# Performance work log

Hardware: AMD Instinct MI355X
Metric: run time of the kernel (lower is better)

## Reference

```python
import jax, jax.numpy as jnp
import numpy as np

VOCAB, EMBED, HIDDEN = 32000, 1024, 1024
BATCH, SEQ = 64, 128
PAD_IDX = 0


def setup_inputs() -> dict:
    key = jax.random.key(0)
    k_in, k_emb, k_wih, k_whh, k_bih, k_bhh = jax.random.split(key, 6)
    inputs = jax.random.randint(k_in, (BATCH, SEQ), 0, VOCAB)
    emb = jax.random.normal(k_emb, (VOCAB, EMBED), dtype=jnp.float32)
    emb = emb.at[PAD_IDX].set(0.0)  # nn.Embedding zeros the padding_idx row
    s = 1.0 / np.sqrt(HIDDEN).astype(np.float32)  # torch LSTMCell init bound
    W_ih = jax.random.uniform(k_wih, (4 * HIDDEN, EMBED), minval=-s, maxval=s, dtype=jnp.float32)
    W_hh = jax.random.uniform(k_whh, (4 * HIDDEN, HIDDEN), minval=-s, maxval=s, dtype=jnp.float32)
    b_ih = jax.random.uniform(k_bih, (4 * HIDDEN,), minval=-s, maxval=s, dtype=jnp.float32)
    b_hh = jax.random.uniform(k_bhh, (4 * HIDDEN,), minval=-s, maxval=s, dtype=jnp.float32)
    return {"emb": emb, "W_ih": W_ih, "W_hh": W_hh, "b_ih": b_ih, "b_hh": b_hh, "inputs": inputs}


def reference(emb, W_ih, W_hh, b_ih, b_hh, inputs):
    # Embedding lookup: [B, S, E] -> time-major [S, B, E]
    x = jnp.swapaxes(emb[inputs], 0, 1)
    B = inputs.shape[0]
    H = W_hh.shape[1]
    h0 = jnp.zeros((B, H), dtype=emb.dtype)
    c0 = jnp.zeros((B, H), dtype=emb.dtype)

    def step(carry, xt):
        h, c = carry
        # torch LSTMCell gate order: i, f, g, o
        gates = xt @ W_ih.T + b_ih + h @ W_hh.T + b_hh  # [B, 4H]
        i, f, g, o = jnp.split(gates, 4, axis=-1)
        i = jax.nn.sigmoid(i)
        f = jax.nn.sigmoid(f)
        g = jnp.tanh(g)
        o = jax.nn.sigmoid(o)
        c2 = f * c + i * g
        h2 = o * jnp.tanh(c2)
        # NOTE: original's h_c_mask is all-zeros (its fill loop only writes
        # zeros), so torch.where always selects the new state -> no masking.
        return (h2, c2), None

    (h, c), _ = jax.lax.scan(step, (h0, c0), x)
    return (h, c)
```

## Files before the change

### kernel.cpp

```cpp
#include <hip/hip_runtime.h>
#include <hip/hip_bf16.h>

#define EMB   1024
#define HID   1024
#define NBATCH 64
#define SEQ   128
#define NGATE 4096
#define NBLK  128

typedef __attribute__((ext_vector_type(8))) short bf16x8;
typedef __attribute__((ext_vector_type(4))) float f32x4;

__device__ __forceinline__ unsigned short f2bf(float f) {
    unsigned int u = __float_as_uint(f);
    unsigned int r = (u + 0x7FFFu + ((u >> 16) & 1u)) >> 16;
    return (unsigned short)r;
}

__device__ __forceinline__ bf16x8 pack8(float4 a, float4 b) {
    bf16x8 r;
    r[0] = (short)f2bf(a.x); r[1] = (short)f2bf(a.y);
    r[2] = (short)f2bf(a.z); r[3] = (short)f2bf(a.w);
    r[4] = (short)f2bf(b.x); r[5] = (short)f2bf(b.y);
    r[6] = (short)f2bf(b.z); r[7] = (short)f2bf(b.w);
    return r;
}

__device__ __forceinline__ float sigmoidf_(float x) { return 1.0f / (1.0f + __expf(-x)); }
__device__ __forceinline__ float tanhf_(float x)    { return 1.0f - 2.0f / (1.0f + __expf(2.0f * x)); }


__global__ void gather_x(const float* __restrict__ emb, const int* __restrict__ inp,
                         unsigned short* __restrict__ xbf) {
    int m = blockIdx.x;
    int t = m >> 6, b = m & 63;
    int tok = inp[b * SEQ + t];
    float4 v = ((const float4*)(emb + (long)tok * EMB))[threadIdx.x];
    ushort4 o;
    o.x = f2bf(v.x); o.y = f2bf(v.y); o.z = f2bf(v.z); o.w = f2bf(v.w);
    ((ushort4*)(xbf + (long)m * EMB))[threadIdx.x] = o;
}

__global__ void conv_w(const float* __restrict__ w, unsigned short* __restrict__ wbf) {
    long i = (long)blockIdx.x * 1024 + (long)threadIdx.x * 4;
    float4 v = *(const float4*)(w + i);
    ushort4 o;
    o.x = f2bf(v.x); o.y = f2bf(v.y); o.z = f2bf(v.z); o.w = f2bf(v.w);
    *(ushort4*)(wbf + i) = o;
}

__global__ void bsum_k(const float* __restrict__ bi, const float* __restrict__ bh,
                       float* __restrict__ bs) {
    int i = blockIdx.x * 256 + threadIdx.x;
    bs[i] = bi[i] + bh[i];
}

__global__ __launch_bounds__(256) void gemm_xw(const unsigned short* __restrict__ A,
                                               const unsigned short* __restrict__ Bw,
                                               const float* __restrict__ bsum,
                                               float* __restrict__ XW) {
    __shared__ unsigned short As[128][40];
    __shared__ unsigned short Bs[128][40];
    int bx = blockIdx.x;
    int by = blockIdx.y;
    int tid = threadIdx.x;
    int w = tid >> 6, l = tid & 63;
    int wm = w >> 1, wn = w & 1;
    int lr = l & 15, lk = l >> 4;

    f32x4 acc[4][4];
#pragma unroll
    for (int ni = 0; ni < 4; ++ni) {
        float bsv = bsum[bx * 128 + wn * 64 + ni * 16 + lr];
#pragma unroll
        for (int mi = 0; mi < 4; ++mi) {
            acc[mi][ni][0] = bsv; acc[mi][ni][1] = bsv;
            acc[mi][ni][2] = bsv; acc[mi][ni][3] = bsv;
        }
    }

    int sr = tid >> 1;
    int sc = (tid & 1) * 16;
    const unsigned short* ga = A  + (long)(by * 128 + sr) * 1024 + sc;
    const unsigned short* gb = Bw + (long)(bx * 128 + sr) * 1024 + sc;

    for (int kt = 0; kt < 32; ++kt) {
        uint4 va0 = *(const uint4*)(ga);
        uint4 va1 = *(const uint4*)(ga + 8);
        uint4 vb0 = *(const uint4*)(gb);
        uint4 vb1 = *(const uint4*)(gb + 8);
        *(uint4*)&As[sr][sc]     = va0;
        *(uint4*)&As[sr][sc + 8] = va1;
        *(uint4*)&Bs[sr][sc]     = vb0;
        *(uint4*)&Bs[sr][sc + 8] = vb1;
        __syncthreads();

        bf16x8 af[4], bfr[4];
#pragma unroll
        for (int mi = 0; mi < 4; ++mi)
            af[mi] = *(const bf16x8*)&As[wm * 64 + mi * 16 + lr][lk * 8];
#pragma unroll
        for (int ni = 0; ni < 4; ++ni)
            bfr[ni] = *(const bf16x8*)&Bs[wn * 64 + ni * 16 + lr][lk * 8];
#pragma unroll
        for (int mi = 0; mi < 4; ++mi)
#pragma unroll
            for (int ni = 0; ni < 4; ++ni)
                acc[mi][ni] = __builtin_amdgcn_mfma_f32_16x16x32_bf16(af[mi], bfr[ni], acc[mi][ni], 0, 0, 0);
        __syncthreads();
        ga += 32; gb += 32;
    }

#pragma unroll
    for (int mi = 0; mi < 4; ++mi) {
        int mg = by * 128 + wm * 64 + mi * 16 + lk * 4;
        int tt = mg >> 6;
        int bb = mg & 63;
#pragma unroll
        for (int ni = 0; ni < 4; ++ni) {
            int nn = bx * 128 + wn * 64 + ni * 16 + lr;
            *(f32x4*)(XW + (long)tt * (NGATE * 64) + (long)nn * 64 + bb) = acc[mi][ni];
        }
    }
}

__global__ __launch_bounds__(512) void lstm_rec(const float* __restrict__ Whh,
                                                const float* __restrict__ XW,
                                                unsigned short* __restrict__ hseq,
                                                unsigned* __restrict__ flags,
                                                float* __restrict__ out) {
    __shared__ float Glds[32][68];
    __shared__ unsigned short Hs[64][8];

    int tid = threadIdx.x;
    int w = tid >> 6, l = tid & 63;
    int lr = l & 15, lk = l >> 4;
    int bg = w & 3, ng = w >> 2;
    int g = blockIdx.x;

    int nl = ng * 16 + lr;
    int q = nl >> 3, u = nl & 7;
    long nrow = (long)(q * 1024 + g * 8 + u) * 1024;
    bf16x8 wf[32];
#pragma unroll
    for (int kk = 0; kk < 32; ++kk) {
        int k0 = kk * 32 + lk * 8;
        float4 w0 = *(const float4*)(Whh + nrow + k0);
        float4 w1 = *(const float4*)(Whh + nrow + k0 + 4);
        wf[kk] = pack8(w0, w1);
    }

    float c = 0.0f;
    int brow = bg * 16 + lr;

    for (int t = 0; t < SEQ; ++t) {
        const uint4* hc = (const uint4*)hseq + (long)t * 8192;

        float px[4];
#pragma unroll
        for (int qq = 0; qq < 4; ++qq)
            px[qq] = XW[(long)t * (NGATE * 64) + (long)(qq * 1024 + g * 8 + w) * 64 + l];

        f32x4 acc0 = {0.f, 0.f, 0.f, 0.f}, acc1 = {0.f, 0.f, 0.f, 0.f};
#pragma unroll
        for (int kk = 0; kk < 32; kk += 2) {
            union { uint4 u4; bf16x8 v; } ua, ub;
            ua.u4 = hc[(kk * 4 + lk) * 64 + brow];
            ub.u4 = hc[((kk + 1) * 4 + lk) * 64 + brow];
            acc0 = __builtin_amdgcn_mfma_f32_16x16x32_bf16(ua.v, wf[kk],     acc0, 0, 0, 0);
            acc1 = __builtin_amdgcn_mfma_f32_16x16x32_bf16(ub.v, wf[kk + 1], acc1, 0, 0, 0);
        }
        f32x4 gacc = acc0 + acc1;
        *(f32x4*)&Glds[ng * 16 + lr][bg * 16 + lk * 4] = gacc;
        __syncthreads();

        float p[4];
#pragma unroll
        for (int qq = 0; qq < 4; ++qq)
            p[qq] = Glds[qq * 8 + w][l] + px[qq];
        float ig = sigmoidf_(p[0]);
        float fg = sigmoidf_(p[1]);
        float gg = tanhf_(p[2]);
        float og = sigmoidf_(p[3]);
        c = fg * c + ig * gg;
        float h = og * tanhf_(c);

        if (t == SEQ - 1) {
            out[l * HID + g * 8 + w] = h;
            out[NBATCH * HID + l * HID + g * 8 + w] = c;
        } else {
            Hs[l][w] = f2bf(h);
            __syncthreads();
            unsigned tv = (unsigned)(t + 1);
            if (tid < 64) {
                unsigned long long* hn = (unsigned long long*)hseq +
                                         (long)(t + 1) * 16384 + (long)g * 128;
                const unsigned long long* hsu = (const unsigned long long*)Hs;
                __hip_atomic_store(&hn[tid * 2],     hsu[tid * 2],
                                   __ATOMIC_RELAXED, __HIP_MEMORY_SCOPE_AGENT);
                __hip_atomic_store(&hn[tid * 2 + 1], hsu[tid * 2 + 1],
                                   __ATOMIC_RELAXED, __HIP_MEMORY_SCOPE_AGENT);
                asm volatile("s_waitcnt vmcnt(0)" ::: "memory");
                if (tid == 0)
                    __hip_atomic_store(&flags[g], tv,
                                       __ATOMIC_RELAXED, __HIP_MEMORY_SCOPE_AGENT);
                if (tid < 32) {
                    const unsigned* fp = flags + tid * 4;
                    long spins = 0;
                    for (;;) {
                        uint4 fv;
                        asm volatile("global_load_dwordx4 %0, %1, off sc0 sc1\n\t"
                                     "s_waitcnt vmcnt(0)"
                                     : "=v"(fv) : "v"(fp) : "memory");
                        unsigned mn = fv.x < fv.y ? fv.x : fv.y;
                        unsigned mn2 = fv.z < fv.w ? fv.z : fv.w;
                        if (mn2 < mn) mn = mn2;
                        if (mn >= tv) break;
                        if (++spins > 500000L) break;
                        __builtin_amdgcn_s_sleep(1);
                    }
                }
            }
            __syncthreads();
        }
    }
}

extern "C" void kernel_launch(void* const* d_in, const int* in_sizes, int n_in,
                              void* d_out, int out_size, void* d_ws, size_t ws_size,
                              hipStream_t stream) {
    const float* emb  = (const float*)d_in[0];
    const float* W_ih = (const float*)d_in[1];
    const float* W_hh = (const float*)d_in[2];
    const float* b_ih = (const float*)d_in[3];
    const float* b_hh = (const float*)d_in[4];
    const int*   inp  = (const int*)d_in[5];
    float* out = (float*)d_out;

    char* ws = (char*)d_ws;
    float*          XW   = (float*)ws;
    unsigned short* Xbf  = (unsigned short*)(ws + 134217728);
    unsigned short* hseq = Xbf;
    unsigned short* Wbf  = (unsigned short*)(ws + 150994944);
    float*          bs   = (float*)(ws + 159383552);
    unsigned*       flags= (unsigned*)(ws + 159399936);

    hipMemsetAsync(flags, 0, NBLK * sizeof(unsigned), stream);
    gather_x<<<SEQ * NBATCH, 256, 0, stream>>>(emb, inp, Xbf);
    conv_w<<<NGATE, 256, 0, stream>>>(W_ih, Wbf);
    bsum_k<<<16, 256, 0, stream>>>(b_ih, b_hh, bs);
    gemm_xw<<<dim3(32, 64), 256, 0, stream>>>(Xbf, Wbf, bs, XW);
    hipMemsetAsync(hseq, 0, NBATCH * HID * sizeof(unsigned short), stream);

    lstm_rec<<<NBLK, 512, 0, stream>>>(W_hh, XW, hseq, flags, out);
}
```

Measured before the change: 1.006 ms.

## Store input projections in bf16, prefetch next step, overlap flag poll with stores

The precomputed input-projection buffer is now written in bf16 instead of fp32, which halves its write and read traffic. The recurrent kernel loads the next timestep's projection values before the barrier spin, so that load is off the critical path. The first flag poll is issued before the flag store and only waits on partial vmcnt, which shortens the per-step synchronization latency. The workspace layout changes so hseq no longer aliases Xbf. Rounding the projections to bf16 adds some error.

```diff
diff --git a/kernel.cpp b/kernel.cpp
--- a/kernel.cpp
+++ b/kernel.cpp
@@ -15,6 +15,10 @@
     unsigned int u = __float_as_uint(f);
     unsigned int r = (u + 0x7FFFu + ((u >> 16) & 1u)) >> 16;
     return (unsigned short)r;
+}
+
+__device__ __forceinline__ float bf2f(unsigned short s) {
+    return __uint_as_float(((unsigned int)s) << 16);
 }
 
 __device__ __forceinline__ bf16x8 pack8(float4 a, float4 b) {
@@ -58,7 +62,7 @@
 __global__ __launch_bounds__(256) void gemm_xw(const unsigned short* __restrict__ A,
                                                const unsigned short* __restrict__ Bw,
                                                const float* __restrict__ bsum,
-                                               float* __restrict__ XW) {
+                                               unsigned short* __restrict__ XWb) {
     __shared__ unsigned short As[128][40];
     __shared__ unsigned short Bs[128][40];
     int bx = blockIdx.x;
@@ -119,13 +123,16 @@
 #pragma unroll
         for (int ni = 0; ni < 4; ++ni) {
             int nn = bx * 128 + wn * 64 + ni * 16 + lr;
-            *(f32x4*)(XW + (long)tt * (NGATE * 64) + (long)nn * 64 + bb) = acc[mi][ni];
+            ushort4 o;
+            o.x = f2bf(acc[mi][ni][0]); o.y = f2bf(acc[mi][ni][1]);
+            o.z = f2bf(acc[mi][ni][2]); o.w = f2bf(acc[mi][ni][3]);
+            *(ushort4*)(XWb + (long)tt * (NGATE * 64) + (long)nn * 64 + bb) = o;
         }
     }
 }
 
 __global__ __launch_bounds__(512) void lstm_rec(const float* __restrict__ Whh,
-                                                const float* __restrict__ XW,
+                                                const unsigned short* __restrict__ XWb,
                                                 unsigned short* __restrict__ hseq,
                                                 unsigned* __restrict__ flags,
                                                 float* __restrict__ out) {
@@ -153,13 +160,13 @@
     float c = 0.0f;
     int brow = bg * 16 + lr;
 
+    unsigned short pxr[4];
+#pragma unroll
+    for (int qq = 0; qq < 4; ++qq)
+        pxr[qq] = XWb[(long)(qq * 1024 + g * 8 + w) * 64 + l];
+
     for (int t = 0; t < SEQ; ++t) {
         const uint4* hc = (const uint4*)hseq + (long)t * 8192;
-
-        float px[4];
-#pragma unroll
-        for (int qq = 0; qq < 4; ++qq)
-            px[qq] = XW[(long)t * (NGATE * 64) + (long)(qq * 1024 + g * 8 + w) * 64 + l];
 
         f32x4 acc0 = {0.f, 0.f, 0.f, 0.f}, acc1 = {0.f, 0.f, 0.f, 0.f};
 #pragma unroll
@@ -177,7 +184,7 @@
         float p[4];
 #pragma unroll
         for (int qq = 0; qq < 4; ++qq)
-            p[qq] = Glds[qq * 8 + w][l] + px[qq];
+            p[qq] = Glds[qq * 8 + w][l] + bf2f(pxr[qq]);
         float ig = sigmoidf_(p[0]);
         float fg = sigmoidf_(p[1]);
         float gg = tanhf_(p[2]);
@@ -191,6 +198,12 @@
         } else {
             Hs[l][w] = f2bf(h);
             __syncthreads();
+
+#pragma unroll
+            for (int qq = 0; qq < 4; ++qq)
+                pxr[qq] = XWb[(long)(t + 1) * (NGATE * 64) +
+                              (long)(qq * 1024 + g * 8 + w) * 64 + l];
+
             unsigned tv = (unsigned)(t + 1);
             if (tid < 64) {
                 unsigned long long* hn = (unsigned long long*)hseq +
@@ -200,25 +213,32 @@
                                    __ATOMIC_RELAXED, __HIP_MEMORY_SCOPE_AGENT);
                 __hip_atomic_store(&hn[tid * 2 + 1], hsu[tid * 2 + 1],
                                    __ATOMIC_RELAXED, __HIP_MEMORY_SCOPE_AGENT);
-                asm volatile("s_waitcnt vmcnt(0)" ::: "memory");
-                if (tid == 0)
-                    __hip_atomic_store(&flags[g], tv,
-                                       __ATOMIC_RELAXED, __HIP_MEMORY_SCOPE_AGENT);
                 if (tid < 32) {
                     const unsigned* fp = flags + tid * 4;
+                    uint4 fv;
+                    asm volatile("global_load_dwordx4 %0, %1, off sc0 sc1"
+                                 : "=v"(fv) : "v"(fp) : "memory");
+                    asm volatile("s_waitcnt vmcnt(1)" ::: "memory");
+                    if (tid == 0)
+                        __hip_atomic_store(&flags[g], tv,
+                                           __ATOMIC_RELAXED, __HIP_MEMORY_SCOPE_AGENT);
+                    asm volatile("s_waitcnt vmcnt(0)" ::: "memory");
+                    __builtin_amdgcn_sched_barrier(0);
                     long spins = 0;
                     for (;;) {
-                        uint4 fv;
-                        asm volatile("global_load_dwordx4 %0, %1, off sc0 sc1\n\t"
-                                     "s_waitcnt vmcnt(0)"
-                                     : "=v"(fv) : "v"(fp) : "memory");
                         unsigned mn = fv.x < fv.y ? fv.x : fv.y;
                         unsigned mn2 = fv.z < fv.w ? fv.z : fv.w;
                         if (mn2 < mn) mn = mn2;
                         if (mn >= tv) break;
                         if (++spins > 500000L) break;
                         __builtin_amdgcn_s_sleep(1);
+                        asm volatile("global_load_dwordx4 %0, %1, off sc0 sc1\n\t"
+                                     "s_waitcnt vmcnt(0)"
+                                     : "=v"(fv) : "v"(fp) : "memory");
+                        __builtin_amdgcn_sched_barrier(0);
                     }
+                } else {
+                    asm volatile("s_waitcnt vmcnt(0)" ::: "memory");
                 }
             }
             __syncthreads();
@@ -238,19 +258,18 @@
     float* out = (float*)d_out;
 
     char* ws = (char*)d_ws;
-    float*          XW   = (float*)ws;
-    unsigned short* Xbf  = (unsigned short*)(ws + 134217728);
-    unsigned short* hseq = Xbf;
-    unsigned short* Wbf  = (unsigned short*)(ws + 150994944);
-    float*          bs   = (float*)(ws + 159383552);
-    unsigned*       flags= (unsigned*)(ws + 159399936);
+    unsigned short* XWb  = (unsigned short*)ws;
+    unsigned short* Xbf  = (unsigned short*)(ws + 67108864);
+    unsigned short* Wbf  = (unsigned short*)(ws + 83886080);
+    float*          bs   = (float*)(ws + 92274688);
+    unsigned short* hseq = (unsigned short*)(ws + 92291072);
+    unsigned*       flags= (unsigned*)(ws + 109068288);
 
     hipMemsetAsync(flags, 0, NBLK * sizeof(unsigned), stream);
+    hipMemsetAsync(hseq, 0, NBATCH * HID * sizeof(unsigned short), stream);
     gather_x<<<SEQ * NBATCH, 256, 0, stream>>>(emb, inp, Xbf);
     conv_w<<<NGATE, 256, 0, stream>>>(W_ih, Wbf);
     bsum_k<<<16, 256, 0, stream>>>(b_ih, b_hh, bs);
-    gemm_xw<<<dim3(32, 64), 256, 0, stream>>>(Xbf, Wbf, bs, XW);
-    hipMemsetAsync(hseq, 0, NBATCH * HID * sizeof(unsigned short), stream);
-
-    lstm_rec<<<NBLK, 512, 0, stream>>>(W_hh, XW, hseq, flags, out);
-}
+    gemm_xw<<<dim3(32, 64), 256, 0, stream>>>(Xbf, Wbf, bs, XWb);
+    lstm_rec<<<NBLK, 512, 0, stream>>>(W_hh, XWb, hseq, flags, out);
+}
```

Result: slower. 1.083 ms (+7.6%).

## Halve recurrent grid to 64 blocks, each handling 16 hidden units

Applied to the files above, without the earlier changes.

The persistent LSTM recurrence kernel now runs on 64 blocks instead of 128. Each block owns 16 hidden units, and each wave covers 32 batch rows with two MFMA accumulator sets. The per-step hidden-state buffer is relaid out as [block][batch][16 units] in its own workspace region, and fewer polling threads check the flags. The aim is to cut the cost of the per-timestep cross-block flag barrier by halving the number of participants, at the price of twice the MFMA and load work per wave on the serial path.

```diff
diff --git a/kernel.cpp b/kernel.cpp
--- a/kernel.cpp
+++ b/kernel.cpp
@@ -6,7 +6,7 @@
 #define NBATCH 64
 #define SEQ   128
 #define NGATE 4096
-#define NBLK  128
+#define NBLK  64
 
 typedef __attribute__((ext_vector_type(8))) short bf16x8;
 typedef __attribute__((ext_vector_type(4))) float f32x4;
@@ -129,18 +129,18 @@
                                                 unsigned short* __restrict__ hseq,
                                                 unsigned* __restrict__ flags,
                                                 float* __restrict__ out) {
-    __shared__ float Glds[32][68];
-    __shared__ unsigned short Hs[64][8];
+    __shared__ float Glds[64][68];
+    __shared__ unsigned short Hs[64][16];
 
     int tid = threadIdx.x;
     int w = tid >> 6, l = tid & 63;
     int lr = l & 15, lk = l >> 4;
-    int bg = w & 3, ng = w >> 2;
+    int bg = w & 1, ng = w >> 1;
     int g = blockIdx.x;
 
     int nl = ng * 16 + lr;
-    int q = nl >> 3, u = nl & 7;
-    long nrow = (long)(q * 1024 + g * 8 + u) * 1024;
+    int q = nl >> 4, uu = nl & 15;
+    long nrow = (long)(q * 1024 + g * 16 + uu) * 1024;
     bf16x8 wf[32];
 #pragma unroll
     for (int kk = 0; kk < 32; ++kk) {
@@ -150,61 +150,83 @@
         wf[kk] = pack8(w0, w1);
     }
 
-    float c = 0.0f;
-    int brow = bg * 16 + lr;
+    float c0 = 0.0f, c1 = 0.0f;
+    int brow = bg * 32 + lr;
+    int sel = lk & 1;
+    int gph = lk >> 1;
 
     for (int t = 0; t < SEQ; ++t) {
         const uint4* hc = (const uint4*)hseq + (long)t * 8192;
 
-        float px[4];
-#pragma unroll
-        for (int qq = 0; qq < 4; ++qq)
-            px[qq] = XW[(long)t * (NGATE * 64) + (long)(qq * 1024 + g * 8 + w) * 64 + l];
-
-        f32x4 acc0 = {0.f, 0.f, 0.f, 0.f}, acc1 = {0.f, 0.f, 0.f, 0.f};
+        float px[2][4];
+#pragma unroll
+        for (int j = 0; j < 2; ++j)
+#pragma unroll
+            for (int qq = 0; qq < 4; ++qq)
+                px[j][qq] = XW[(long)t * (NGATE * 64) +
+                               (long)(qq * 1024 + g * 16 + w + j * 8) * 64 + l];
+
+        f32x4 aA0 = {0.f,0.f,0.f,0.f}, aA1 = {0.f,0.f,0.f,0.f};
+        f32x4 aB0 = {0.f,0.f,0.f,0.f}, aB1 = {0.f,0.f,0.f,0.f};
 #pragma unroll
         for (int kk = 0; kk < 32; kk += 2) {
-            union { uint4 u4; bf16x8 v; } ua, ub;
-            ua.u4 = hc[(kk * 4 + lk) * 64 + brow];
-            ub.u4 = hc[((kk + 1) * 4 + lk) * 64 + brow];
-            acc0 = __builtin_amdgcn_mfma_f32_16x16x32_bf16(ua.v, wf[kk],     acc0, 0, 0, 0);
-            acc1 = __builtin_amdgcn_mfma_f32_16x16x32_bf16(ub.v, wf[kk + 1], acc1, 0, 0, 0);
-        }
-        f32x4 gacc = acc0 + acc1;
-        *(f32x4*)&Glds[ng * 16 + lr][bg * 16 + lk * 4] = gacc;
+            int gp0 = kk * 2 + gph;
+            int gp1 = (kk + 1) * 2 + gph;
+            union { uint4 u4; bf16x8 v; } ua, ub, uc, ud;
+            ua.u4 = hc[(gp0 * 64 + brow) * 2 + sel];
+            ub.u4 = hc[(gp1 * 64 + brow) * 2 + sel];
+            uc.u4 = hc[(gp0 * 64 + brow + 16) * 2 + sel];
+            ud.u4 = hc[(gp1 * 64 + brow + 16) * 2 + sel];
+            aA0 = __builtin_amdgcn_mfma_f32_16x16x32_bf16(ua.v, wf[kk],     aA0, 0, 0, 0);
+            aA1 = __builtin_amdgcn_mfma_f32_16x16x32_bf16(ub.v, wf[kk + 1], aA1, 0, 0, 0);
+            aB0 = __builtin_amdgcn_mfma_f32_16x16x32_bf16(uc.v, wf[kk],     aB0, 0, 0, 0);
+            aB1 = __builtin_amdgcn_mfma_f32_16x16x32_bf16(ud.v, wf[kk + 1], aB1, 0, 0, 0);
+        }
+        f32x4 gA = aA0 + aA1, gB = aB0 + aB1;
+        *(f32x4*)&Glds[nl][bg * 32 + lk * 4]      = gA;
+        *(f32x4*)&Glds[nl][bg * 32 + 16 + lk * 4] = gB;
         __syncthreads();
 
-        float p[4];
-#pragma unroll
-        for (int qq = 0; qq < 4; ++qq)
-            p[qq] = Glds[qq * 8 + w][l] + px[qq];
-        float ig = sigmoidf_(p[0]);
-        float fg = sigmoidf_(p[1]);
-        float gg = tanhf_(p[2]);
-        float og = sigmoidf_(p[3]);
-        c = fg * c + ig * gg;
-        float h = og * tanhf_(c);
+        float hv[2], cv[2] = {c0, c1};
+#pragma unroll
+        for (int j = 0; j < 2; ++j) {
+            float p[4];
+#pragma unroll
+            for (int qq = 0; qq < 4; ++qq)
+                p[qq] = Glds[qq * 16 + w + j * 8][l] + px[j][qq];
+            float ig = sigmoidf_(p[0]);
+            float fg = sigmoidf_(p[1]);
+            float gg = tanhf_(p[2]);
+            float og = sigmoidf_(p[3]);
+            cv[j] = fg * cv[j] + ig * gg;
+            hv[j] = og * tanhf_(cv[j]);
+        }
+        c0 = cv[0]; c1 = cv[1];
 
         if (t == SEQ - 1) {
-            out[l * HID + g * 8 + w] = h;
-            out[NBATCH * HID + l * HID + g * 8 + w] = c;
+            out[l * HID + g * 16 + w]     = hv[0];
+            out[l * HID + g * 16 + w + 8] = hv[1];
+            out[NBATCH * HID + l * HID + g * 16 + w]     = c0;
+            out[NBATCH * HID + l * HID + g * 16 + w + 8] = c1;
         } else {
-            Hs[l][w] = f2bf(h);
+            Hs[l][w]     = f2bf(hv[0]);
+            Hs[l][w + 8] = f2bf(hv[1]);
             __syncthreads();
             unsigned tv = (unsigned)(t + 1);
+
             if (tid < 64) {
                 unsigned long long* hn = (unsigned long long*)hseq +
-                                         (long)(t + 1) * 16384 + (long)g * 128;
+                                         (long)(t + 1) * 16384 + (long)g * 256;
                 const unsigned long long* hsu = (const unsigned long long*)Hs;
-                __hip_atomic_store(&hn[tid * 2],     hsu[tid * 2],
-                                   __ATOMIC_RELAXED, __HIP_MEMORY_SCOPE_AGENT);
-                __hip_atomic_store(&hn[tid * 2 + 1], hsu[tid * 2 + 1],
-                                   __ATOMIC_RELAXED, __HIP_MEMORY_SCOPE_AGENT);
+#pragma unroll
+                for (int s = 0; s < 4; ++s)
+                    __hip_atomic_store(&hn[tid * 4 + s], hsu[tid * 4 + s],
+                                       __ATOMIC_RELAXED, __HIP_MEMORY_SCOPE_AGENT);
                 asm volatile("s_waitcnt vmcnt(0)" ::: "memory");
                 if (tid == 0)
                     __hip_atomic_store(&flags[g], tv,
                                        __ATOMIC_RELAXED, __HIP_MEMORY_SCOPE_AGENT);
-                if (tid < 32) {
+                if (tid < 16) {
                     const unsigned* fp = flags + tid * 4;
                     long spins = 0;
                     for (;;) {
@@ -212,7 +234,8 @@
                         asm volatile("global_load_dwordx4 %0, %1, off sc0 sc1\n\t"
                                      "s_waitcnt vmcnt(0)"
                                      : "=v"(fv) : "v"(fp) : "memory");
-                        unsigned mn = fv.x < fv.y ? fv.x : fv.y;
+                        __builtin_amdgcn_sched_barrier(0);
+                        unsigned mn  = fv.x < fv.y ? fv.x : fv.y;
                         unsigned mn2 = fv.z < fv.w ? fv.z : fv.w;
                         if (mn2 < mn) mn = mn2;
                         if (mn >= tv) break;
@@ -240,17 +263,16 @@
     char* ws = (char*)d_ws;
     float*          XW   = (float*)ws;
     unsigned short* Xbf  = (unsigned short*)(ws + 134217728);
-    unsigned short* hseq = Xbf;
     unsigned short* Wbf  = (unsigned short*)(ws + 150994944);
     float*          bs   = (float*)(ws + 159383552);
-    unsigned*       flags= (unsigned*)(ws + 159399936);
+    unsigned short* hseq = (unsigned short*)(ws + 159399936);
+    unsigned*       flags= (unsigned*)(ws + 176177152);
 
     hipMemsetAsync(flags, 0, NBLK * sizeof(unsigned), stream);
+    hipMemsetAsync(hseq, 0, NBATCH * HID * sizeof(unsigned short), stream);
     gather_x<<<SEQ * NBATCH, 256, 0, stream>>>(emb, inp, Xbf);
     conv_w<<<NGATE, 256, 0, stream>>>(W_ih, Wbf);
     bsum_k<<<16, 256, 0, stream>>>(b_ih, b_hh, bs);
     gemm_xw<<<dim3(32, 64), 256, 0, stream>>>(Xbf, Wbf, bs, XW);
-    hipMemsetAsync(hseq, 0, NBATCH * HID * sizeof(unsigned short), stream);
-
     lstm_rec<<<NBLK, 512, 0, stream>>>(W_hh, XW, hseq, flags, out);
 }
```

Result: slower. 1.311 ms (+30.3%).

## Replace flat grid barrier with two-level hierarchical flag barrier

Applied to the files above, without the earlier changes.

The per-step grid barrier used to have 32 lanes in every block poll all 128 flags. It now works in two levels: one leader block per group of eight polls only its group's eight flags, then writes a group-done flag into 16 replicated slots. Every block then polls only its own replica of the 16 group flags, which cuts the polling traffic on shared cache lines. The change also moves hseq into its own workspace region instead of aliasing Xbf, and zeroes it up front, in exchange for an extra hop of barrier latency.

```diff
diff --git a/kernel.cpp b/kernel.cpp
--- a/kernel.cpp
+++ b/kernel.cpp
@@ -137,6 +137,11 @@
     int lr = l & 15, lk = l >> 4;
     int bg = w & 3, ng = w >> 2;
     int g = blockIdx.x;
+    unsigned* flags1 = flags;
+    unsigned* flags2 = flags + 128;
+    int grp = g >> 3;
+    int rep = g & 15;
+    bool leader = (g & 7) == 0;
 
     int nl = ng * 16 + lr;
     int q = nl >> 3, u = nl & 7;
@@ -159,7 +164,8 @@
         float px[4];
 #pragma unroll
         for (int qq = 0; qq < 4; ++qq)
-            px[qq] = XW[(long)t * (NGATE * 64) + (long)(qq * 1024 + g * 8 + w) * 64 + l];
+            px[qq] = XW[(long)t * (NGATE * 64) +
+                        (long)(qq * 1024 + g * 8 + w) * 64 + l];
 
         f32x4 acc0 = {0.f, 0.f, 0.f, 0.f}, acc1 = {0.f, 0.f, 0.f, 0.f};
 #pragma unroll
@@ -192,6 +198,7 @@
             Hs[l][w] = f2bf(h);
             __syncthreads();
             unsigned tv = (unsigned)(t + 1);
+
             if (tid < 64) {
                 unsigned long long* hn = (unsigned long long*)hseq +
                                          (long)(t + 1) * 16384 + (long)g * 128;
@@ -202,17 +209,42 @@
                                    __ATOMIC_RELAXED, __HIP_MEMORY_SCOPE_AGENT);
                 asm volatile("s_waitcnt vmcnt(0)" ::: "memory");
                 if (tid == 0)
-                    __hip_atomic_store(&flags[g], tv,
+                    __hip_atomic_store(&flags1[g], tv,
                                        __ATOMIC_RELAXED, __HIP_MEMORY_SCOPE_AGENT);
-                if (tid < 32) {
-                    const unsigned* fp = flags + tid * 4;
+
+                if (leader) {
+                    if (tid < 2) {
+                        const unsigned* fp = flags1 + g + tid * 4;
+                        long spins = 0;
+                        for (;;) {
+                            uint4 fv;
+                            asm volatile("global_load_dwordx4 %0, %1, off sc0 sc1\n\t"
+                                         "s_waitcnt vmcnt(0)"
+                                         : "=v"(fv) : "v"(fp) : "memory");
+                            __builtin_amdgcn_sched_barrier(0);
+                            unsigned mn  = fv.x < fv.y ? fv.x : fv.y;
+                            unsigned mn2 = fv.z < fv.w ? fv.z : fv.w;
+                            if (mn2 < mn) mn = mn2;
+                            if (mn >= tv) break;
+                            if (++spins > 500000L) break;
+                            __builtin_amdgcn_s_sleep(1);
+                        }
+                    }
+                    if (tid < 16)
+                        __hip_atomic_store(&flags2[tid * 16 + grp], tv,
+                                           __ATOMIC_RELAXED, __HIP_MEMORY_SCOPE_AGENT);
+                }
+
+                if (tid < 4) {
+                    const unsigned* fp = flags2 + rep * 16 + tid * 4;
                     long spins = 0;
                     for (;;) {
                         uint4 fv;
                         asm volatile("global_load_dwordx4 %0, %1, off sc0 sc1\n\t"
                                      "s_waitcnt vmcnt(0)"
                                      : "=v"(fv) : "v"(fp) : "memory");
-                        unsigned mn = fv.x < fv.y ? fv.x : fv.y;
+                        __builtin_amdgcn_sched_barrier(0);
+                        unsigned mn  = fv.x < fv.y ? fv.x : fv.y;
                         unsigned mn2 = fv.z < fv.w ? fv.z : fv.w;
                         if (mn2 < mn) mn = mn2;
                         if (mn >= tv) break;
@@ -240,17 +272,16 @@
     char* ws = (char*)d_ws;
     float*          XW   = (float*)ws;
     unsigned short* Xbf  = (unsigned short*)(ws + 134217728);
-    unsigned short* hseq = Xbf;
     unsigned short* Wbf  = (unsigned short*)(ws + 150994944);
     float*          bs   = (float*)(ws + 159383552);
-    unsigned*       flags= (unsigned*)(ws + 159399936);
-
-    hipMemsetAsync(flags, 0, NBLK * sizeof(unsigned), stream);
+    unsigned short* hseq = (unsigned short*)(ws + 159399936);
+    unsigned*       flags= (unsigned*)(ws + 176177152);
+
+    hipMemsetAsync(flags, 0, 1536, stream);
+    hipMemsetAsync(hseq, 0, NBATCH * HID * sizeof(unsigned short), stream);
     gather_x<<<SEQ * NBATCH, 256, 0, stream>>>(emb, inp, Xbf);
     conv_w<<<NGATE, 256, 0, stream>>>(W_ih, Wbf);
     bsum_k<<<16, 256, 0, stream>>>(b_ih, b_hh, bs);
     gemm_xw<<<dim3(32, 64), 256, 0, stream>>>(Xbf, Wbf, bs, XW);
-    hipMemsetAsync(hseq, 0, NBATCH * HID * sizeof(unsigned short), stream);
-
     lstm_rec<<<NBLK, 512, 0, stream>>>(W_hh, XW, hseq, flags, out);
 }
```

New measurement: 813.3 us (median of 2 runs). -19.2%, faster.
